# Kernel optimization log

Measured on AMD Instinct MI355X. Metric: run time of the kernel, lower is better.

Reference implementation:

```python
import jax, jax.numpy as jnp
import numpy as np
from jax import lax

V, E, H, T = 100000, 256, 256, 8192
FL, FN, NC = 5, 128, 20


def setup_inputs() -> dict:
    key = jax.random.key(0)
    ks = jax.random.split(key, 12)
    s = 0.05
    return {
        "docs": jax.random.randint(ks[0], (1, T), 0, V),
        "docs_length": jnp.array([T]),
        "labels": jax.random.randint(ks[1], (1,), 0, NC),
        "iteration": 0,
        "embed_W": jax.random.uniform(ks[2], (V, E), jnp.float32, -0.1, 0.1),
        "w_ih": jax.random.normal(ks[3], (4 * H, E), jnp.float32) * s,
        "w_hh": jax.random.normal(ks[4], (4 * H, H), jnp.float32) * s,
        "b_ih": jax.random.normal(ks[5], (4 * H,), jnp.float32) * s,
        "b_hh": jax.random.normal(ks[6], (4 * H,), jnp.float32) * s,
        "conv_w": jax.random.normal(ks[7], (FN, 1, FL, H), jnp.float32) * s,
        "conv_b": jax.random.normal(ks[8], (FN,), jnp.float32) * s,
        "logits_w": jax.random.uniform(ks[9], (NC, FN), jnp.float32, -0.1, 0.1),
        "logits_b": jnp.zeros((NC,), jnp.float32),
    }


def _forward(docs, labels, embed_W, w_ih, w_hh, b_ih, b_hh, conv_w, conv_b, logits_w, logits_b):
    # embed -> ReLU (dropout is identity at p=0)
    x = jax.nn.relu(embed_W[docs[0]])  # (T, E)

    b = b_ih + b_hh

    def step(carry, xt):
        h, c = carry
        g = xt @ w_ih.T + h @ w_hh.T + b  # (4H,)
        i, f, gg, o = jnp.split(g, 4)
        i = jax.nn.sigmoid(i)
        f = jax.nn.sigmoid(f)
        gg = jnp.tanh(gg)
        o = jax.nn.sigmoid(o)
        c = f * c + i * gg
        h = o * jnp.tanh(c)
        return (h, c), h

    init = (jnp.zeros((H,), x.dtype), jnp.zeros((H,), x.dtype))
    _, hs = lax.scan(step, init, x)  # (T, H)

    # Conv2d(1, FN, (FL, H)) valid: (1,1,T,H) -> (1,FN,T-FL+1,1)
    feat = lax.conv_general_dilated(
        hs[None, None, :, :], conv_w, window_strides=(1, 1), padding="VALID",
        dimension_numbers=("NCHW", "OIHW", "NCHW"))
    feat = feat[0, :, :, 0] + conv_b[:, None]  # (FN, T-FL+1)

    # AdaptiveMaxPool2d((FN,1)) == max over time
    pooled = jnp.max(feat, axis=1)  # (FN,)

    logits = pooled @ logits_w.T + logits_b  # (NC,)
    logp = jax.nn.log_softmax(logits)
    loss = -logp[labels[0]]
    acc = (jnp.argmax(logp) == labels[0]).astype(jnp.float32)
    return loss, acc


def reference(docs, docs_length, labels, iteration, embed_W, w_ih, w_hh, b_ih, b_hh,
              conv_w, conv_b, logits_w, logits_b):
    return _forward(docs, labels, embed_W, w_ih, w_hh, b_ih, b_hh,
                    conv_w, conv_b, logits_w, logits_b)
```

## Files before the change

kernel.cpp:

```cpp
#include <hip/hip_runtime.h>
#include <math.h>

#define T_LEN 8192

typedef float f32x4 __attribute__((ext_vector_type(4)));
typedef int   i32x8 __attribute__((ext_vector_type(8)));

#define DPP_MAX(x, ctrl) fmaxf((x), __int_as_float(__builtin_amdgcn_update_dpp(0, __float_as_int(x), (ctrl), 0xF, 0xF, true)))

#define BAR_LDS() do { \
    __builtin_amdgcn_sched_barrier(0); \
    asm volatile("s_waitcnt lgkmcnt(0)" ::: "memory"); \
    __builtin_amdgcn_s_barrier(); \
    __builtin_amdgcn_sched_barrier(0); \
} while (0)

__device__ __forceinline__ float fsig(float x) {
    float e = __expf(-x);
    return __builtin_amdgcn_rcpf(1.f + e);
}
__device__ __forceinline__ float fsig_c(float x) {
    x = fminf(30.f, fmaxf(-30.f, x));
    float e = __expf(-x);
    return __builtin_amdgcn_rcpf(1.f + e);
}
__device__ __forceinline__ float ftanh_c(float x) {
    x = fminf(15.f, fmaxf(-15.f, x));
    float e = __expf(-2.f * x);
    return (1.f - e) * __builtin_amdgcn_rcpf(1.f + e);
}

__device__ __forceinline__ unsigned char enc_e4m3(float x) {
#if __has_builtin(__builtin_amdgcn_cvt_pk_fp8_f32)
    int v = __builtin_amdgcn_cvt_pk_fp8_f32(x, 0.f, 0, false);
    return (unsigned char)(v & 0xff);
#else
    unsigned u = __float_as_uint(x);
    unsigned s = (u >> 24) & 0x80u;
    float a = fabsf(x);
    if (a > 448.f) a = 448.f;
    if (a < 9.765625e-4f) return (unsigned char)s;
    int e = ((int)((__float_as_uint(a) >> 23) & 0xffu)) - 127;
    int eu = e < -6 ? -6 : e;
    float ulp = exp2f((float)(eu - 3));
    float q = rintf(a / ulp);
    int mant, ee;
    if (eu == -6 && q < 8.f) { mant = (int)q; ee = 0; }
    else {
        if (q >= 16.f) { q *= 0.5f; eu += 1; }
        mant = (int)q - 8; ee = eu + 7;
        if (ee > 15 || (ee == 15 && mant > 6)) { ee = 15; mant = 6; }
    }
    return (unsigned char)(s | (unsigned)(ee << 3) | (unsigned)mant);
#endif
}
__device__ __forceinline__ unsigned pk4(float a, float b, float c, float d) {
    return (unsigned)enc_e4m3(a) | ((unsigned)enc_e4m3(b) << 8)
         | ((unsigned)enc_e4m3(c) << 16) | ((unsigned)enc_e4m3(d) << 24);
}

__device__ __forceinline__ unsigned enc_e2m3(float x) {
    unsigned s = (__float_as_uint(x) >> 31) << 5;
    float a = fabsf(x);
    a = fminf(a, 7.5f);
    if (a < 0.0625f) return s;
    int e = ((int)((__float_as_uint(a) >> 23) & 0xffu)) - 127;
    int eu = e < 0 ? 0 : e;
    float ulp = __int_as_float((unsigned)(eu + 124) << 23);
    float q = rintf(a * __builtin_amdgcn_rcpf(ulp));
    int E, M;
    if (e < 0) {
        if (q >= 8.f) { E = 1; M = 0; }
        else { E = 0; M = (int)q; }
    } else {
        if (q >= 16.f) { q = 8.f; eu += 1; }
        if (eu > 2) { E = 3; M = 7; }
        else { E = eu + 1; M = (int)q - 8; }
    }
    return s | (unsigned)(E << 3) | (unsigned)M;
}

__device__ __forceinline__ int enc_e2m3_h4(float h) {
    float x = h * 4.f;
    float a = fabsf(x);
    int c1 = (int)rintf(a * 8.f);
    int c2 = (int)rintf(a * 4.f) + 8;
    int mag = (a < 2.f) ? c1 : c2;
    return mag | (int)((__float_as_uint(h) >> 26) & 32u);
}

__global__ __launch_bounds__(256) void pack_w6(
    const float* __restrict__ w_hh,
    unsigned* __restrict__ w6)
{
    int idx = blockIdx.x * 256 + threadIdx.x;
    int l  = idx & 63;
    int kt = (idx >> 6) & 1;
    int gt = idx >> 7;
    int rw = l & 15, kg = l >> 4;
    int rowp = (gt << 4) + rw;
    int orow = ((rowp & 3) << 8) + (rowp >> 2);
    const float* s = w_hh + (size_t)orow * 256 + 128 * kt + 32 * kg;
    unsigned d[6] = {0, 0, 0, 0, 0, 0};
#pragma unroll
    for (int j = 0; j < 32; ++j) {
        unsigned c = enc_e2m3(s[j] * 32.f);
        int bit = 6 * j;
        d[bit >> 5] |= c << (bit & 31);
        if ((bit & 31) > 26) d[(bit >> 5) + 1] |= c >> (32 - (bit & 31));
    }
    unsigned* o = w6 + (size_t)idx * 8;
    o[0] = d[0]; o[1] = d[1]; o[2] = d[2];
    o[3] = d[3]; o[4] = d[4]; o[5] = d[5];
    o[6] = 0;    o[7] = 0;
}

__global__ __launch_bounds__(256, 4) void gemm_pre(
    const int* __restrict__ docs,
    const float* __restrict__ embW,
    const float* __restrict__ w_ih,
    const float* __restrict__ b_ih,
    const float* __restrict__ b_hh,
    float* __restrict__ pre)
{
    __shared__ __align__(16) float As[16][68];
    __shared__ __align__(16) float Bs[16][68];
    __shared__ int rowid[64];
    const int bt = blockIdx.x;
    const int bj = blockIdx.y;
    const int tid = threadIdx.x;
    if (tid < 64) rowid[tid] = docs[bt * 64 + tid];
    __syncthreads();
    const int ti = tid & 15, tj = tid >> 4;
    const int r = tid & 63;
    const int kk4 = (tid >> 6) * 4;
    float acc[4][4];
#pragma unroll
    for (int ii = 0; ii < 4; ++ii)
#pragma unroll
        for (int jj = 0; jj < 4; ++jj) acc[ii][jj] = 0.f;

    for (int k0 = 0; k0 < 256; k0 += 16) {
        float4 av = *(const float4*)(embW + (size_t)rowid[r] * 256 + k0 + kk4);
        float4 bv = *(const float4*)(w_ih + (size_t)(bj * 64 + r) * 256 + k0 + kk4);
        As[kk4 + 0][r] = fmaxf(av.x, 0.f);
        As[kk4 + 1][r] = fmaxf(av.y, 0.f);
        As[kk4 + 2][r] = fmaxf(av.z, 0.f);
        As[kk4 + 3][r] = fmaxf(av.w, 0.f);
        Bs[kk4 + 0][r] = bv.x;
        Bs[kk4 + 1][r] = bv.y;
        Bs[kk4 + 2][r] = bv.z;
        Bs[kk4 + 3][r] = bv.w;
        __syncthreads();
#pragma unroll
        for (int kk = 0; kk < 16; ++kk) {
            float4 a = *(const float4*)&As[kk][ti * 4];
            float4 b = *(const float4*)&Bs[kk][tj * 4];
            acc[0][0] += a.x * b.x; acc[0][1] += a.x * b.y; acc[0][2] += a.x * b.z; acc[0][3] += a.x * b.w;
            acc[1][0] += a.y * b.x; acc[1][1] += a.y * b.y; acc[1][2] += a.y * b.z; acc[1][3] += a.y * b.w;
            acc[2][0] += a.z * b.x; acc[2][1] += a.z * b.y; acc[2][2] += a.z * b.z; acc[2][3] += a.z * b.w;
            acc[3][0] += a.w * b.x; acc[3][1] += a.w * b.y; acc[3][2] += a.w * b.z; acc[3][3] += a.w * b.w;
        }
        __syncthreads();
    }
#pragma unroll
    for (int ii = 0; ii < 4; ++ii) {
        int t = bt * 64 + ti * 4 + ii;
#pragma unroll
        for (int jj = 0; jj < 4; ++jj) {
            int j = bj * 64 + tj * 4 + jj;
            int jp = ((j & 255) << 2) | (j >> 8);
            pre[(size_t)t * 1024 + jp] = acc[ii][jj] + b_ih[j] + b_hh[j];
        }
    }
}

__global__ __launch_bounds__(256, 1) void lstm_scan_mx6w4(
    const float* __restrict__ pre,
    const unsigned* __restrict__ w6,
    float* __restrict__ hs)
{
    const int tid = threadIdx.x;
    const int w  = tid >> 6;
    const int l  = tid & 63;
    const int rto = l & 15;
    const int kg  = l >> 4;
    const float INV = 1.f / 128.f;

    __shared__ __align__(16) unsigned char h6pk[2][256];

    i32x8 wA[16][2];
#pragma unroll
    for (int rtt = 0; rtt < 16; ++rtt) {
#pragma unroll
        for (int kt = 0; kt < 2; ++kt) {
            int gt = 16 * w + rtt;
            const unsigned* s = w6 + (size_t)((gt * 2 + kt) * 64 + l) * 8;
            uint4 lo = *(const uint4*)s;
            uint2 hi = *(const uint2*)(s + 4);
            i32x8 v;
            v[0] = (int)lo.x; v[1] = (int)lo.y; v[2] = (int)lo.z;
            v[3] = (int)lo.w; v[4] = (int)hi.x; v[5] = (int)hi.y;
            v[6] = 0; v[7] = 0;
            wA[rtt][kt] = v;
        }
    }

    for (int i = tid; i < 512; i += 256) ((unsigned char*)h6pk)[i] = 0;

    const int u = 64 * w + 4 * rto + kg;
    float c_st = 0.f;

    const bool b0 = (rto & 1), b1 = (rto & 2), b2 = (rto & 4), b3 = (rto & 8);

    const bool iswr = (l < 48);
    const int s_  = (l >= 24) ? 1 : 0;
    const int b_  = l - 24 * s_;
    const int j0  = (4 * b_) / 3;
    const int rsh = 8 * b_ - 6 * j0;
    const int j1  = j0 + 1;
    const int lj0 = 16 * (j0 & 3) + 8 * s_ + (j0 >> 2);
    const int lj1 = 16 * (j1 & 3) + 8 * s_ + (j1 >> 2);
    const int wofs = (2 * w + s_) * 32 + b_;

    int rd_par = 256;
    int wr_par = 0;

    i32x8 bq0 = (i32x8){0, 0, 0, 0, 0, 0, 0, 0};
    i32x8 bq1 = (i32x8){0, 0, 0, 0, 0, 0, 0, 0};

    f32x4 p4c = *(const f32x4*)(pre + 4 * u);
    const float* pp = pre + 1024 + 4 * u;
    float* hsp = hs + u;
    const unsigned char* h6base = (const unsigned char*)h6pk;
    BAR_LDS();

    for (int t = 0; t < T_LEN; ++t) {
        f32x4 p4n = *(const f32x4*)pp;
        pp += 1024;

        {
            const unsigned char* bp0 = h6base + rd_par + kg * 32;
            uint4 lo = *(const uint4*)bp0;
            uint2 hi = *(const uint2*)(bp0 + 16);
            bq0[0] = (int)lo.x; bq0[1] = (int)lo.y; bq0[2] = (int)lo.z;
            bq0[3] = (int)lo.w; bq0[4] = (int)hi.x; bq0[5] = (int)hi.y;
            const unsigned char* bp1 = bp0 + 128;
            uint4 lo1 = *(const uint4*)bp1;
            uint2 hi1 = *(const uint2*)(bp1 + 16);
            bq1[0] = (int)lo1.x; bq1[1] = (int)lo1.y; bq1[2] = (int)lo1.z;
            bq1[3] = (int)lo1.w; bq1[4] = (int)hi1.x; bq1[5] = (int)hi1.y;
        }

        f32x4 acc[16];
#pragma unroll
        for (int rtt = 0; rtt < 16; ++rtt) {
            acc[rtt] = __builtin_amdgcn_mfma_scale_f32_16x16x128_f8f6f4(
                wA[rtt][0], bq0, (f32x4){0.f, 0.f, 0.f, 0.f},
                2, 2, 0, 0x7f7f7f7f, 0, 0x7f7f7f7f);
            acc[rtt] = __builtin_amdgcn_mfma_scale_f32_16x16x128_f8f6f4(
                wA[rtt][1], bq1, acc[rtt],
                2, 2, 0, 0x7f7f7f7f, 0, 0x7f7f7f7f);
        }

        f32x4 s0 = b0 ? acc[1]  : acc[0];
        f32x4 s1 = b0 ? acc[3]  : acc[2];
        f32x4 s2 = b0 ? acc[5]  : acc[4];
        f32x4 s3 = b0 ? acc[7]  : acc[6];
        f32x4 s4 = b0 ? acc[9]  : acc[8];
        f32x4 s5 = b0 ? acc[11] : acc[10];
        f32x4 s6 = b0 ? acc[13] : acc[12];
        f32x4 s7 = b0 ? acc[15] : acc[14];
        f32x4 q0 = b1 ? s1 : s0;
        f32x4 q1 = b1 ? s3 : s2;
        f32x4 q2 = b1 ? s5 : s4;
        f32x4 q3 = b1 ? s7 : s6;
        f32x4 r0 = b2 ? q1 : q0;
        f32x4 r1 = b2 ? q3 : q2;
        f32x4 av = b3 ? r1 : r0;

        float gi = fmaf(av.x, INV, p4c.x);
        float gf = fmaf(av.y, INV, p4c.y);
        float gg = fmaf(av.z, INV, p4c.z);
        float go = fmaf(av.w, INV, p4c.w);
        float si = fsig(gi);
        float sf = fsig(gf);
        float tg = 2.f * fsig(2.f * gg) - 1.f;
        float so = fsig(go);
        c_st = sf * c_st + si * tg;
        float h = so * (2.f * fsig(2.f * c_st) - 1.f);
        hsp[0] = h;
        hsp += 256;
        int code = enc_e2m3_h4(h);

        int c0 = __shfl(code, lj0, 64);
        int c1 = __shfl(code, lj1, 64);
        if (iswr) {
            unsigned byte = (((unsigned)c0 >> rsh) | ((unsigned)c1 << (6 - rsh))) & 0xffu;
            *((unsigned char*)h6pk + wr_par + wofs) = (unsigned char)byte;
        }

        p4c = p4n;
        rd_par ^= 256;
        wr_par ^= 256;
        BAR_LDS();
    }
}

__global__ __launch_bounds__(512, 2) void lstm_scan_mx6(
    const float* __restrict__ pre,
    const unsigned* __restrict__ w6,
    float* __restrict__ hs)
{
    const int tid = threadIdx.x;
    const int w  = tid >> 6;
    const int l  = tid & 63;
    const int rw = l & 15;
    const int kg = l >> 4;
    const float INV = 1.f / 128.f;

    __shared__ __align__(16) unsigned char h6pk[2][256];
    __shared__ __align__(16) float ldsPre[2][1024];

    i32x8 wA[8][2];
#pragma unroll
    for (int rt = 0; rt < 8; ++rt) {
#pragma unroll
        for (int kt = 0; kt < 2; ++kt) {
            const unsigned* s = w6 + (size_t)(((w * 8 + rt) * 2 + kt) * 64 + l) * 8;
            uint4 lo = *(const uint4*)s;
            uint2 hi = *(const uint2*)(s + 4);
            i32x8 v;
            v[0] = (int)lo.x; v[1] = (int)lo.y; v[2] = (int)lo.z;
            v[3] = (int)lo.w; v[4] = (int)hi.x; v[5] = (int)hi.y;
            v[6] = 0; v[7] = 0;
            wA[rt][kt] = v;
        }
    }

    for (int i = tid; i < 512; i += 512) h6pk[0][i] = 0;
    {
        float2 p = *(const float2*)(pre + 2 * tid);
        *(float2*)&ldsPre[0][2 * tid] = p;
    }

    const bool isup = (rw < 8);
    const int u = 32 * w + 4 * (rw & 7) + kg;
    float c_st = 0.f;

    const bool iswr = (rw < 8) && (kg < 3);
    const int bby = 8 * kg + rw;
    const int j0  = (4 * bby) / 3;
    const int rsh = 8 * bby - 6 * j0;
    const int lj0 = 16 * (j0 & 3) + (j0 >> 2);
    const int j1  = j0 + 1;
    const int lj1 = 16 * (j1 & 3) + (j1 >> 2);

    const float* pnext = pre + 1024 + 2 * tid;
    float* hsp = hs + u;
    __syncthreads();

    for (int t = 0; t < T_LEN; ++t) {
        const int PW = t & 1;
        const int PR = PW ^ 1;

        f32x4 p4 = *(const f32x4*)&ldsPre[PW][4 * u];

        float2 pv = *(const float2*)pnext;
        if (t + 2 < T_LEN) pnext += 1024;

        i32x8 bq[2];
#pragma unroll
        for (int kt = 0; kt < 2; ++kt) {
            const unsigned char* bp = &h6pk[PR][(4 * kt + kg) * 32];
            uint4 lo = *(const uint4*)bp;
            uint2 hi = *(const uint2*)(bp + 16);
            i32x8 b;
            b[0] = (int)lo.x; b[1] = (int)lo.y; b[2] = (int)lo.z; b[3] = (int)lo.w;
            b[4] = (int)hi.x; b[5] = (int)hi.y; b[6] = 0; b[7] = 0;
            bq[kt] = b;
        }

        f32x4 acc[8];
#pragma unroll
        for (int rt = 0; rt < 8; ++rt) acc[rt] = (f32x4){0.f, 0.f, 0.f, 0.f};
#pragma unroll
        for (int rt = 0; rt < 8; ++rt)
#pragma unroll
            for (int kt = 0; kt < 2; ++kt)
                acc[rt] = __builtin_amdgcn_mfma_scale_f32_16x16x128_f8f6f4(
                    wA[rt][kt], bq[kt], acc[rt],
                    2, 2, 0, 0x7f7f7f7f, 0, 0x7f7f7f7f);

        int code = 0;
        if (isup) {
            f32x4 av = acc[0];
            av = (rw == 1) ? acc[1] : av;
            av = (rw == 2) ? acc[2] : av;
            av = (rw == 3) ? acc[3] : av;
            av = (rw == 4) ? acc[4] : av;
            av = (rw == 5) ? acc[5] : av;
            av = (rw == 6) ? acc[6] : av;
            av = (rw == 7) ? acc[7] : av;
            float gi = fmaf(av.x, INV, p4.x);
            float gf = fmaf(av.y, INV, p4.y);
            float gg = fmaf(av.z, INV, p4.z);
            float go = fmaf(av.w, INV, p4.w);
            float si = fsig_c(gi);
            float sf = fsig_c(gf);
            float tg = ftanh_c(gg);
            float so = fsig_c(go);
            c_st = sf * c_st + si * tg;
            float h = so * ftanh_c(c_st);
            hsp[0] = h;
            code = (int)enc_e2m3(h * 4.f);
        }
        hsp += 256;

        int c0 = __shfl(code, lj0, 64);
        int c1 = __shfl(code, lj1, 64);
        if (iswr) {
            unsigned byte = (((unsigned)c0 >> rsh) | ((unsigned)c1 << (6 - rsh))) & 0xffu;
            h6pk[PW][w * 32 + bby] = (unsigned char)byte;
        }

        *(float2*)&ldsPre[PR][2 * tid] = pv;

        __syncthreads();
    }
}

__global__ __launch_bounds__(512, 2) void lstm_scan_mx8(
    const float* __restrict__ pre,
    const float* __restrict__ w_hh,
    float* __restrict__ hs)
{
    const int tid = threadIdx.x;
    const int w  = tid >> 6;
    const int l  = tid & 63;
    const int rw = l & 15;
    const int kg = l >> 4;
    const float INV = 1.f / 32768.f;

    __shared__ __align__(16) unsigned char h8[2 * 256];
    __shared__ __align__(16) float ldsPre[2][1024];

    i32x8 wA[8][2];
#pragma unroll
    for (int rt = 0; rt < 8; ++rt) {
#pragma unroll
        for (int kt = 0; kt < 2; ++kt) {
            int rowp = ((8 * w + rt) << 4) + rw;
            int orow = ((rowp & 3) << 8) + (rowp >> 2);
            const float* s = w_hh + (size_t)orow * 256 + 128 * kt + 32 * kg;
            i32x8 v;
#pragma unroll
            for (int d = 0; d < 8; ++d) {
                float4 f = *(const float4*)(s + 4 * d);
                v[d] = (int)pk4(f.x * 512.f, f.y * 512.f, f.z * 512.f, f.w * 512.f);
            }
            wA[rt][kt] = v;
        }
    }

    for (int i = tid; i < 512; i += 512) h8[i] = 0;
    {
        float2 p = *(const float2*)(pre + 2 * tid);
        *(float2*)&ldsPre[0][2 * tid] = p;
    }
    float c_st = 0.f;
    const bool isup = (rw < 8);
    const int u = 32 * w + 4 * (rw & 7) + kg;
    const float* pnext = pre + 1024 + 2 * tid;
    float* hsp = hs + u;
    __syncthreads();

    for (int t = 0; t < T_LEN; ++t) {
        const int PW = t & 1;
        const int PR = PW ^ 1;

        f32x4 p4 = *(const f32x4*)&ldsPre[PW][4 * u];

        float2 pv = *(const float2*)pnext;
        if (t + 2 < T_LEN) pnext += 1024;

        i32x8 bq[2];
#pragma unroll
        for (int kt = 0; kt < 2; ++kt) {
            const unsigned char* bp = &h8[PR * 256 + 128 * kt + 32 * kg];
            uint4 lo = *(const uint4*)bp;
            uint4 hi = *(const uint4*)(bp + 16);
            i32x8 b;
            b[0] = (int)lo.x; b[1] = (int)lo.y; b[2] = (int)lo.z; b[3] = (int)lo.w;
            b[4] = (int)hi.x; b[5] = (int)hi.y; b[6] = (int)hi.z; b[7] = (int)hi.w;
            bq[kt] = b;
        }

        f32x4 acc[8];
#pragma unroll
        for (int rt = 0; rt < 8; ++rt) acc[rt] = (f32x4){0.f, 0.f, 0.f, 0.f};
#pragma unroll
        for (int rt = 0; rt < 8; ++rt)
#pragma unroll
            for (int kt = 0; kt < 2; ++kt)
                acc[rt] = __builtin_amdgcn_mfma_scale_f32_16x16x128_f8f6f4(
                    wA[rt][kt], bq[kt], acc[rt],
                    0, 0, 0, 0x7f7f7f7f, 0, 0x7f7f7f7f);

        if (isup) {
            f32x4 av = acc[0];
            av = (rw == 1) ? acc[1] : av;
            av = (rw == 2) ? acc[2] : av;
            av = (rw == 3) ? acc[3] : av;
            av = (rw == 4) ? acc[4] : av;
            av = (rw == 5) ? acc[5] : av;
            av = (rw == 6) ? acc[6] : av;
            av = (rw == 7) ? acc[7] : av;
            float gi = fmaf(av.x, INV, p4.x);
            float gf = fmaf(av.y, INV, p4.y);
            float gg = fmaf(av.z, INV, p4.z);
            float go = fmaf(av.w, INV, p4.w);
            float si = fsig_c(gi);
            float sf = fsig_c(gf);
            float tg = ftanh_c(gg);
            float so = fsig_c(go);
            c_st = sf * c_st + si * tg;
            float h = so * ftanh_c(c_st);
            hsp[0] = h;
            h8[PW * 256 + u] = enc_e4m3(h * 64.f);
        }
        hsp += 256;

        *(float2*)&ldsPre[PR][2 * tid] = pv;

        __syncthreads();
    }
}

__global__ __launch_bounds__(256) void conv_pool(
    const float* __restrict__ hs,
    const float* __restrict__ cw,
    const float* __restrict__ cb,
    float* __restrict__ part)
{
    __shared__ __align__(16) float hst[68 * 260];
    __shared__ __align__(16) float cwS[128 * 68];
    const int blk = blockIdx.x;
    const int t0 = blk * 64;
    const int tid = threadIdx.x;
    const int i = tid & 15;
    const int g = tid >> 4;

    for (int e = tid; e < 68 * 64; e += 256) {
        int rr = e >> 6;
        int c4 = (e & 63) * 4;
        int tg = t0 + rr; if (tg > 8191) tg = 8191;
        float4 v = *(const float4*)(hs + (size_t)tg * 256 + c4);
        *(float4*)&hst[rr * 260 + c4] = v;
    }

    float acc[4][8];
#pragma unroll
    for (int tt = 0; tt < 4; ++tt)
#pragma unroll
        for (int j = 0; j < 8; ++j) acc[tt][j] = 0.f;

    for (int l = 0; l < 5; ++l) {
        for (int hc = 0; hc < 4; ++hc) {
            __syncthreads();
            {
                int n = tid >> 1;
                int hb = (tid & 1) * 32;
                const float* src = cw + (size_t)n * 1280 + l * 256 + hc * 64 + hb;
                float* dst = &cwS[n * 68 + hb];
#pragma unroll
                for (int q = 0; q < 8; ++q) {
                    float4 v = *(const float4*)(src + 4 * q);
                    *(float4*)(dst + 4 * q) = v;
                }
            }
            __syncthreads();
#pragma unroll 4
            for (int q = 0; q < 16; ++q) {
                float4 hvv[4];
#pragma unroll
                for (int tt = 0; tt < 4; ++tt)
                    hvv[tt] = *(const float4*)&hst[(i + 16 * tt + l) * 260 + hc * 64 + 4 * q];
#pragma unroll
                for (int j = 0; j < 8; ++j) {
                    float4 wv = *(const float4*)&cwS[(g + 16 * j) * 68 + 4 * q];
#pragma unroll
                    for (int tt = 0; tt < 4; ++tt) {
                        acc[tt][j] += hvv[tt].x * wv.x + hvv[tt].y * wv.y
                                    + hvv[tt].z * wv.z + hvv[tt].w * wv.w;
                    }
                }
            }
        }
    }

    float m[8];
#pragma unroll
    for (int j = 0; j < 8; ++j) {
        int n = g + 16 * j;
        float cbn = cb[n];
        float mm = -INFINITY;
#pragma unroll
        for (int tt = 0; tt < 4; ++tt) {
            int t = t0 + i + 16 * tt;
            float v = acc[tt][j] + cbn;
            if (t < 8188) mm = fmaxf(mm, v);
        }
        mm = DPP_MAX(mm, 0xB1);
        mm = DPP_MAX(mm, 0x4E);
        mm = DPP_MAX(mm, 0x141);
        mm = DPP_MAX(mm, 0x140);
        m[j] = mm;
    }
    if (i == 0) {
#pragma unroll
        for (int j = 0; j < 8; ++j)
            part[(size_t)blk * 128 + g + 16 * j] = m[j];
    }
}

__global__ void final_head(
    const float* __restrict__ part,
    const float* __restrict__ logits_w,
    const float* __restrict__ logits_b,
    const int* __restrict__ labels,
    float* __restrict__ out)
{
    __shared__ float pooled[128];
    __shared__ float lgt[20];
    int tid = threadIdx.x;
    float mx = -INFINITY;
    for (int b = 0; b < 128; ++b) mx = fmaxf(mx, part[(size_t)b * 128 + tid]);
    pooled[tid] = mx;
    __syncthreads();
    if (tid < 20) {
        float s = logits_b[tid];
        for (int k = 0; k < 128; ++k) s += logits_w[tid * 128 + k] * pooled[k];
        lgt[tid] = s;
    }
    __syncthreads();
    if (tid == 0) {
        float m = lgt[0]; int am = 0;
        for (int c2 = 1; c2 < 20; ++c2) { if (lgt[c2] > m) { m = lgt[c2]; am = c2; } }
        float se = 0.f;
        for (int c2 = 0; c2 < 20; ++c2) se += expf(lgt[c2] - m);
        float lse = m + logf(se);
        int lbl = labels[0];
        out[0] = -(lgt[lbl] - lse);
        out[1] = (am == lbl) ? 1.f : 0.f;
    }
}

extern "C" void kernel_launch(void* const* d_in, const int* in_sizes, int n_in,
                              void* d_out, int out_size, void* d_ws, size_t ws_size,
                              hipStream_t stream) {
    (void)in_sizes; (void)n_in; (void)out_size;
    const int*   docs   = (const int*)d_in[0];
    const int*   labels = (const int*)d_in[2];
    const float* embW   = (const float*)d_in[4];
    const float* w_ih   = (const float*)d_in[5];
    const float* w_hh   = (const float*)d_in[6];
    const float* b_ih   = (const float*)d_in[7];
    const float* b_hh   = (const float*)d_in[8];
    const float* cw     = (const float*)d_in[9];
    const float* cb     = (const float*)d_in[10];
    const float* lw     = (const float*)d_in[11];
    const float* lb     = (const float*)d_in[12];
    float* out = (float*)d_out;

    char* ws = (char*)d_ws;
    float*    pre  = (float*)(ws);
    float*    hs   = (float*)(ws + 33554432);
    float*    part = (float*)(ws + 41943040);
    unsigned* w6   = (unsigned*)(ws + 42008576);

    bool ws_ok = (ws_size >= (size_t)42270720);
    hipFuncAttributes a4, a6;
    bool ok4 = ws_ok
        && (hipFuncGetAttributes(&a4, (const void*)lstm_scan_mx6w4) == hipSuccess)
        && (a4.localSizeBytes == 0);
    bool ok6 = ws_ok
        && (hipFuncGetAttributes(&a6, (const void*)lstm_scan_mx6) == hipSuccess)
        && (a6.localSizeBytes == 0);

    gemm_pre<<<dim3(128, 16, 1), 256, 0, stream>>>(docs, embW, w_ih, b_ih, b_hh, pre);
    if (ok4 || ok6) {
        pack_w6<<<32, 256, 0, stream>>>(w_hh, w6);
        if (ok4) lstm_scan_mx6w4<<<1, 256, 0, stream>>>(pre, w6, hs);
        else     lstm_scan_mx6<<<1, 512, 0, stream>>>(pre, w6, hs);
    } else {
        lstm_scan_mx8<<<1, 512, 0, stream>>>(pre, w_hh, hs);
    }
    conv_pool<<<128, 256, 0, stream>>>(hs, cw, cb, part);
    final_head<<<1, 128, 0, stream>>>(part, lw, lb, labels, out);
}
```

Baseline: 5.956 ms.

## Hold recurrent weights in AGPRs via inline-asm MFMA and prefold exp2 constants

The LSTM scan kernel now issues the scaled FP6 MFMA pairs through inline assembly so the weight operands live in AGPRs as 6-dword vectors rather than padded 8-dword VGPR vectors. This frees VGPRs and avoids spilling, at the cost of a fixed s_nop hazard wait that is hand-inserted after the MFMAs. The sigmoid and tanh now use exp2 with the log2(e) factors folded into the precomputed input projection and the 1/128 scale, which removes multiplies from the serial critical path. The time loop is also unrolled by two so the double-buffer offsets become constants.

```diff
diff --git a/kernel.cpp b/kernel.cpp
--- a/kernel.cpp
+++ b/kernel.cpp
@@ -5,6 +5,7 @@
 
 typedef float f32x4 __attribute__((ext_vector_type(4)));
 typedef int   i32x8 __attribute__((ext_vector_type(8)));
+typedef int   i32x6 __attribute__((ext_vector_type(6)));
 
 #define DPP_MAX(x, ctrl) fmaxf((x), __int_as_float(__builtin_amdgcn_update_dpp(0, __float_as_int(x), (ctrl), 0xF, 0xF, true)))
 
@@ -15,8 +16,14 @@
     __builtin_amdgcn_sched_barrier(0); \
 } while (0)
 
-__device__ __forceinline__ float fsig(float x) {
-    float e = __expf(-x);
+__device__ __forceinline__ float fexp2(float x) {
+#if __has_builtin(__builtin_amdgcn_exp2f)
+    return __builtin_amdgcn_exp2f(x);
+#else
+    return exp2f(x);
+#endif
+}
+__device__ __forceinline__ float rcp1p(float e) {
     return __builtin_amdgcn_rcpf(1.f + e);
 }
 __device__ __forceinline__ float fsig_c(float x) {
@@ -175,7 +182,13 @@
     }
 }
 
-__global__ __launch_bounds__(256, 1) void lstm_scan_mx6w4(
+#define MFMA_PAIR(RT, DST) \
+    asm("v_mfma_scale_f32_16x16x128_f8f6f4 %0, %1, %2, %5, %6, %6 cbsz:2 blgp:2\n\t" \
+        "v_mfma_scale_f32_16x16x128_f8f6f4 %0, %3, %4, %0, %6, %6 cbsz:2 blgp:2" \
+        : "=&v"(DST) \
+        : "a"(wA[RT][0]), "v"(bq0), "a"(wA[RT][1]), "v"(bq1), "v"(CZ), "v"(sc))
+
+__global__ __launch_bounds__(256, 1) void lstm_scan_mx6a(
     const float* __restrict__ pre,
     const unsigned* __restrict__ w6,
     float* __restrict__ hs)
@@ -185,11 +198,14 @@
     const int l  = tid & 63;
     const int rto = l & 15;
     const int kg  = l >> 4;
-    const float INV = 1.f / 128.f;
-
-    __shared__ __align__(16) unsigned char h6pk[2][256];
-
-    i32x8 wA[16][2];
+    const float C_L2E  = -1.4426950408889634f;
+    const float C_L2E2 = -2.8853900817779268f;
+    const float I_L2E  = C_L2E  / 128.f;
+    const float I_L2E2 = C_L2E2 / 128.f;
+
+    __shared__ __align__(32) unsigned char h6pk[2][256];
+
+    i32x6 wA[16][2];
 #pragma unroll
     for (int rtt = 0; rtt < 16; ++rtt) {
 #pragma unroll
@@ -198,10 +214,9 @@
             const unsigned* s = w6 + (size_t)((gt * 2 + kt) * 64 + l) * 8;
             uint4 lo = *(const uint4*)s;
             uint2 hi = *(const uint2*)(s + 4);
-            i32x8 v;
+            i32x6 v;
             v[0] = (int)lo.x; v[1] = (int)lo.y; v[2] = (int)lo.z;
             v[3] = (int)lo.w; v[4] = (int)hi.x; v[5] = (int)hi.y;
-            v[6] = 0; v[7] = 0;
             wA[rtt][kt] = v;
         }
     }
@@ -223,88 +238,83 @@
     const int lj1 = 16 * (j1 & 3) + 8 * s_ + (j1 >> 2);
     const int wofs = (2 * w + s_) * 32 + b_;
 
-    int rd_par = 256;
-    int wr_par = 0;
-
-    i32x8 bq0 = (i32x8){0, 0, 0, 0, 0, 0, 0, 0};
-    i32x8 bq1 = (i32x8){0, 0, 0, 0, 0, 0, 0, 0};
+    f32x4 CZ = (f32x4){0.f, 0.f, 0.f, 0.f};
+    asm("" : "+v"(CZ));
+    int sc = 0x7f7f7f7f;
 
     f32x4 p4c = *(const f32x4*)(pre + 4 * u);
+    float tx = p4c.x * C_L2E;
+    float ty = p4c.y * C_L2E;
+    float tz = p4c.z * C_L2E2;
+    float tw = p4c.w * C_L2E;
     const float* pp = pre + 1024 + 4 * u;
     float* hsp = hs + u;
     const unsigned char* h6base = (const unsigned char*)h6pk;
     BAR_LDS();
 
-    for (int t = 0; t < T_LEN; ++t) {
-        f32x4 p4n = *(const f32x4*)pp;
-        pp += 1024;
-
-        {
-            const unsigned char* bp0 = h6base + rd_par + kg * 32;
-            uint4 lo = *(const uint4*)bp0;
-            uint2 hi = *(const uint2*)(bp0 + 16);
-            bq0[0] = (int)lo.x; bq0[1] = (int)lo.y; bq0[2] = (int)lo.z;
-            bq0[3] = (int)lo.w; bq0[4] = (int)hi.x; bq0[5] = (int)hi.y;
-            const unsigned char* bp1 = bp0 + 128;
-            uint4 lo1 = *(const uint4*)bp1;
-            uint2 hi1 = *(const uint2*)(bp1 + 16);
-            bq1[0] = (int)lo1.x; bq1[1] = (int)lo1.y; bq1[2] = (int)lo1.z;
-            bq1[3] = (int)lo1.w; bq1[4] = (int)hi1.x; bq1[5] = (int)hi1.y;
-        }
-
-        f32x4 acc[16];
-#pragma unroll
-        for (int rtt = 0; rtt < 16; ++rtt) {
-            acc[rtt] = __builtin_amdgcn_mfma_scale_f32_16x16x128_f8f6f4(
-                wA[rtt][0], bq0, (f32x4){0.f, 0.f, 0.f, 0.f},
-                2, 2, 0, 0x7f7f7f7f, 0, 0x7f7f7f7f);
-            acc[rtt] = __builtin_amdgcn_mfma_scale_f32_16x16x128_f8f6f4(
-                wA[rtt][1], bq1, acc[rtt],
-                2, 2, 0, 0x7f7f7f7f, 0, 0x7f7f7f7f);
-        }
-
-        f32x4 s0 = b0 ? acc[1]  : acc[0];
-        f32x4 s1 = b0 ? acc[3]  : acc[2];
-        f32x4 s2 = b0 ? acc[5]  : acc[4];
-        f32x4 s3 = b0 ? acc[7]  : acc[6];
-        f32x4 s4 = b0 ? acc[9]  : acc[8];
-        f32x4 s5 = b0 ? acc[11] : acc[10];
-        f32x4 s6 = b0 ? acc[13] : acc[12];
-        f32x4 s7 = b0 ? acc[15] : acc[14];
-        f32x4 q0 = b1 ? s1 : s0;
-        f32x4 q1 = b1 ? s3 : s2;
-        f32x4 q2 = b1 ? s5 : s4;
-        f32x4 q3 = b1 ? s7 : s6;
-        f32x4 r0 = b2 ? q1 : q0;
-        f32x4 r1 = b2 ? q3 : q2;
-        f32x4 av = b3 ? r1 : r0;
-
-        float gi = fmaf(av.x, INV, p4c.x);
-        float gf = fmaf(av.y, INV, p4c.y);
-        float gg = fmaf(av.z, INV, p4c.z);
-        float go = fmaf(av.w, INV, p4c.w);
-        float si = fsig(gi);
-        float sf = fsig(gf);
-        float tg = 2.f * fsig(2.f * gg) - 1.f;
-        float so = fsig(go);
-        c_st = sf * c_st + si * tg;
-        float h = so * (2.f * fsig(2.f * c_st) - 1.f);
-        hsp[0] = h;
-        hsp += 256;
-        int code = enc_e2m3_h4(h);
-
-        int c0 = __shfl(code, lj0, 64);
-        int c1 = __shfl(code, lj1, 64);
-        if (iswr) {
-            unsigned byte = (((unsigned)c0 >> rsh) | ((unsigned)c1 << (6 - rsh))) & 0xffu;
-            *((unsigned char*)h6pk + wr_par + wofs) = (unsigned char)byte;
-        }
-
-        p4c = p4n;
-        rd_par ^= 256;
-        wr_par ^= 256;
-        BAR_LDS();
-    }
+#define LSTM_STEP(RD, WR) do { \
+    f32x4 p4n = *(const f32x4*)pp; pp += 1024; \
+    i32x6 bq0, bq1; \
+    { \
+        const unsigned char* bp0 = h6base + (RD) + kg * 32; \
+        uint4 lo = *(const uint4*)bp0; \
+        uint2 hi = *(const uint2*)(bp0 + 16); \
+        bq0[0] = (int)lo.x; bq0[1] = (int)lo.y; bq0[2] = (int)lo.z; \
+        bq0[3] = (int)lo.w; bq0[4] = (int)hi.x; bq0[5] = (int)hi.y; \
+        const unsigned char* bp1 = bp0 + 128; \
+        uint4 lo1 = *(const uint4*)bp1; \
+        uint2 hi1 = *(const uint2*)(bp1 + 16); \
+        bq1[0] = (int)lo1.x; bq1[1] = (int)lo1.y; bq1[2] = (int)lo1.z; \
+        bq1[3] = (int)lo1.w; bq1[4] = (int)hi1.x; bq1[5] = (int)hi1.y; \
+    } \
+    f32x4 a0, a1, a2, a3, a4, a5, a6, a7, a8, a9, a10, a11, a12, a13, a14, a15; \
+    MFMA_PAIR(0, a0);  MFMA_PAIR(1, a1);  MFMA_PAIR(2, a2);  MFMA_PAIR(3, a3); \
+    MFMA_PAIR(4, a4);  MFMA_PAIR(5, a5);  MFMA_PAIR(6, a6);  MFMA_PAIR(7, a7); \
+    MFMA_PAIR(8, a8);  MFMA_PAIR(9, a9);  MFMA_PAIR(10, a10); MFMA_PAIR(11, a11); \
+    MFMA_PAIR(12, a12); MFMA_PAIR(13, a13); MFMA_PAIR(14, a14); MFMA_PAIR(15, a15); \
+    asm volatile("s_nop 7\n\ts_nop 7\n\ts_nop 7" \
+        : "+v"(a0), "+v"(a1), "+v"(a2), "+v"(a3), "+v"(a4), "+v"(a5), "+v"(a6), "+v"(a7), \
+          "+v"(a8), "+v"(a9), "+v"(a10), "+v"(a11), "+v"(a12), "+v"(a13), "+v"(a14), "+v"(a15)); \
+    f32x4 s0 = b0 ? a1  : a0; \
+    f32x4 s1 = b0 ? a3  : a2; \
+    f32x4 s2 = b0 ? a5  : a4; \
+    f32x4 s3 = b0 ? a7  : a6; \
+    f32x4 s4 = b0 ? a9  : a8; \
+    f32x4 s5 = b0 ? a11 : a10; \
+    f32x4 s6 = b0 ? a13 : a12; \
+    f32x4 s7 = b0 ? a15 : a14; \
+    f32x4 q0 = b1 ? s1 : s0; \
+    f32x4 q1 = b1 ? s3 : s2; \
+    f32x4 q2 = b1 ? s5 : s4; \
+    f32x4 q3 = b1 ? s7 : s6; \
+    f32x4 r0 = b2 ? q1 : q0; \
+    f32x4 r1 = b2 ? q3 : q2; \
+    f32x4 av = b3 ? r1 : r0; \
+    float nx = p4n.x * C_L2E, ny = p4n.y * C_L2E; \
+    float nz = p4n.z * C_L2E2, nw = p4n.w * C_L2E; \
+    float si = rcp1p(fexp2(fmaf(av.x, I_L2E,  tx))); \
+    float sf = rcp1p(fexp2(fmaf(av.y, I_L2E,  ty))); \
+    float tg = 2.f * rcp1p(fexp2(fmaf(av.z, I_L2E2, tz))) - 1.f; \
+    float so = rcp1p(fexp2(fmaf(av.w, I_L2E,  tw))); \
+    c_st = sf * c_st + si * tg; \
+    float h = so * (2.f * rcp1p(fexp2(c_st * C_L2E2)) - 1.f); \
+    hsp[0] = h; hsp += 256; \
+    int code = enc_e2m3_h4(h); \
+    int c0 = __shfl(code, lj0, 64); \
+    int c1 = __shfl(code, lj1, 64); \
+    if (iswr) { \
+        unsigned byte = (((unsigned)c0 >> rsh) | ((unsigned)c1 << (6 - rsh))) & 0xffu; \
+        *((unsigned char*)h6pk + (WR) + wofs) = (unsigned char)byte; \
+    } \
+    tx = nx; ty = ny; tz = nz; tw = nw; \
+    BAR_LDS(); \
+} while (0)
+
+    for (int t2 = 0; t2 < T_LEN; t2 += 2) {
+        LSTM_STEP(256, 0);
+        LSTM_STEP(0, 256);
+    }
+#undef LSTM_STEP
 }
 
 __global__ __launch_bounds__(512, 2) void lstm_scan_mx6(
@@ -680,18 +690,18 @@
     unsigned* w6   = (unsigned*)(ws + 42008576);
 
     bool ws_ok = (ws_size >= (size_t)42270720);
-    hipFuncAttributes a4, a6;
-    bool ok4 = ws_ok
-        && (hipFuncGetAttributes(&a4, (const void*)lstm_scan_mx6w4) == hipSuccess)
-        && (a4.localSizeBytes == 0);
+    hipFuncAttributes aA, a6;
+    bool okA = ws_ok
+        && (hipFuncGetAttributes(&aA, (const void*)lstm_scan_mx6a) == hipSuccess)
+        && (aA.localSizeBytes == 0);
     bool ok6 = ws_ok
         && (hipFuncGetAttributes(&a6, (const void*)lstm_scan_mx6) == hipSuccess)
         && (a6.localSizeBytes == 0);
 
     gemm_pre<<<dim3(128, 16, 1), 256, 0, stream>>>(docs, embW, w_ih, b_ih, b_hh, pre);
-    if (ok4 || ok6) {
+    if (okA || ok6) {
         pack_w6<<<32, 256, 0, stream>>>(w_hh, w6);
-        if (ok4) lstm_scan_mx6w4<<<1, 256, 0, stream>>>(pre, w6, hs);
+        if (okA) lstm_scan_mx6a<<<1, 256, 0, stream>>>(pre, w6, hs);
         else     lstm_scan_mx6<<<1, 512, 0, stream>>>(pre, w6, hs);
     } else {
         lstm_scan_mx8<<<1, 512, 0, stream>>>(pre, w_hh, hs);
```

New measurement: 5.519 ms. 1.08x faster.
